# Optimization experiments

Measured on AMD Instinct MI355X. Metric: run time of the kernel, lower is better.

Reference implementation:

```python
import jax, jax.numpy as jnp
import numpy as np

N_NODES = 100000
IN_DIM = 128
HID_DIM = 128
N_EDGES = 1600000
BN_EPS = 1e-5


def setup_inputs() -> dict:
    key = jax.random.key(0)
    k1, k2, k3, k4 = jax.random.split(key, 4)
    x = jax.random.normal(k1, (N_NODES, IN_DIM), dtype=jnp.float32)
    edge_index = jax.random.randint(k2, (2, N_EDGES), 0, N_NODES, dtype=jnp.int64)
    # GCNConv linear weight (glorot) and bias
    W = jax.random.normal(k3, (HID_DIM, IN_DIM), dtype=jnp.float32) * (1.0 / np.sqrt(IN_DIM))
    b = jnp.zeros((HID_DIM,), dtype=jnp.float32)
    # BatchNorm affine params
    gamma = jnp.ones((HID_DIM,), dtype=jnp.float32)
    beta = jnp.zeros((HID_DIM,), dtype=jnp.float32)
    return {"x": x, "edge_index": edge_index, "W": W, "b": b, "gamma": gamma, "beta": beta}


def reference(x, edge_index, W, b, gamma, beta):
    n = x.shape[0]
    # --- GCNConv: add self loops, symmetric normalization ---
    loops = jnp.arange(n, dtype=edge_index.dtype)
    row = jnp.concatenate([edge_index[0], loops])  # source j
    col = jnp.concatenate([edge_index[1], loops])  # target i
    deg = jax.ops.segment_sum(jnp.ones_like(col, dtype=x.dtype), col, num_segments=n)
    deg_inv_sqrt = jnp.where(deg > 0, jax.lax.rsqrt(jnp.maximum(deg, 1e-12)), 0.0)
    norm = deg_inv_sqrt[row] * deg_inv_sqrt[col]  # [E+N]
    # linear transform then normalized gather-scatter aggregation
    h = x @ W.T  # [N, H]
    msgs = h[row] * norm[:, None]  # [E+N, H]
    out = jax.ops.segment_sum(msgs, col, num_segments=n) + b  # [N, H]
    # --- BatchNorm1d (training-mode batch stats, biased var) + ReLU ---
    mean = jnp.mean(out, axis=0)
    var = jnp.mean(jnp.square(out - mean), axis=0)
    out = (out - mean) * jax.lax.rsqrt(var + BN_EPS) * gamma + beta
    return jax.nn.relu(out)
```

## Files before the change

### kernel.cpp

```cpp
#include <hip/hip_runtime.h>

#define N_NODES 100000
#define N_EDGES 1600000
#define BN_EPS 1e-5f
#define SB 25
#define SCAP 69632
#define NBB 800
#define CAP 2688

typedef short short8 __attribute__((ext_vector_type(8)));
typedef float floatx4 __attribute__((ext_vector_type(4)));

__device__ __forceinline__ unsigned short f2bf(float f) {
    unsigned int u = __float_as_uint(f);
    unsigned int r = (u + 0x7fffu + ((u >> 16) & 1u)) >> 16;
    return (unsigned short)r;
}
__device__ __forceinline__ float bflo(unsigned int v) { return __uint_as_float(v << 16); }
__device__ __forceinline__ float bfhi(unsigned int v) { return __uint_as_float(v & 0xffff0000u); }

__global__ __launch_bounds__(512) void k_binA(const int* __restrict__ ei,
                                              int* __restrict__ scnt,
                                              unsigned int* __restrict__ b1, int E) {
    __shared__ int hist[32], base[32], gbase[32];
    __shared__ unsigned int stage[4096];
    __shared__ unsigned char stb[4096];
    int tid = threadIdx.x;
    int e0 = blockIdx.x * 4096;
    int cn = min(4096, E - e0);
    if (tid < 32) hist[tid] = 0;
    __syncthreads();

    unsigned int mycode[8];
    short myslot[8];
    signed char myb[8];
    #pragma unroll
    for (int j = 0; j < 8; j++) {
        int idx = j * 512 + tid;
        if (idx < cn) {
            int src = ei[e0 + idx];
            int dst = ei[E + e0 + idx];
            int s = dst >> 12;
            mycode[j] = (unsigned int)src | ((unsigned int)(dst & 4095) << 17);
            myb[j] = (signed char)s;
            myslot[j] = (short)atomicAdd(&hist[s], 1);
        } else myb[j] = -1;
    }
    __syncthreads();
    if (tid == 0) {
        int run = 0;
        for (int s = 0; s < SB; s++) { base[s] = run; run += hist[s]; }
    }
    __syncthreads();
    #pragma unroll
    for (int j = 0; j < 8; j++) {
        if (myb[j] >= 0) {
            int p = base[myb[j]] + myslot[j];
            stage[p] = mycode[j];
            stb[p] = (unsigned char)myb[j];
        }
    }
    if (tid < SB && hist[tid]) gbase[tid] = tid * SCAP + atomicAdd(&scnt[tid], hist[tid]);
    __syncthreads();
    for (int i = tid; i < cn; i += 512) {
        int s = stb[i];
        b1[gbase[s] + (i - base[s])] = stage[i];
    }
}

__global__ __launch_bounds__(512) void k_binB(const unsigned int* __restrict__ b1,
                                              const int* __restrict__ scnt,
                                              int* __restrict__ bcnt,
                                              unsigned int* __restrict__ b2) {
    __shared__ int hist[32], base[32], gbase[32];
    __shared__ unsigned int stage[4096];
    __shared__ unsigned char stb[4096];
    int tid = threadIdx.x;
    int s = blockIdx.x / 17;
    int c = blockIdx.x % 17;
    int cnt = scnt[s];
    int e0 = s * SCAP + c * 4096;
    int cn = min(4096, cnt - c * 4096);
    if (tid < 32) hist[tid] = 0;
    __syncthreads();

    unsigned int mycode[8];
    short myslot[8];
    signed char myb[8];
    #pragma unroll
    for (int j = 0; j < 8; j++) {
        int idx = j * 512 + tid;
        if (idx < cn) {
            unsigned int code = b1[e0 + idx];
            int sub = (code >> 24) & 31;
            mycode[j] = code & 0x00FFFFFFu;
            myb[j] = (signed char)sub;
            myslot[j] = (short)atomicAdd(&hist[sub], 1);
        } else myb[j] = -1;
    }
    __syncthreads();
    if (tid == 0) {
        int run = 0;
        for (int k = 0; k < 32; k++) { base[k] = run; run += hist[k]; }
    }
    __syncthreads();
    #pragma unroll
    for (int j = 0; j < 8; j++) {
        if (myb[j] >= 0) {
            int p = base[myb[j]] + myslot[j];
            stage[p] = mycode[j];
            stb[p] = (unsigned char)myb[j];
        }
    }
    if (tid < 32 && hist[tid]) {
        int gb = s * 32 + tid;
        gbase[tid] = gb * CAP + atomicAdd(&bcnt[gb], hist[tid]);
    }
    __syncthreads();
    for (int i = tid; i < cn; i += 512) {
        int sub = stb[i];
        b2[gbase[sub] + (i - base[sub])] = stage[i];
    }
}

__global__ __launch_bounds__(256) void k_dd(const unsigned int* __restrict__ binned,
                                            const int* __restrict__ bcnt,
                                            float* __restrict__ dinv, int n) {
    __shared__ int hist[128];
    int b = blockIdx.x, t = threadIdx.x;
    int nb0 = b * 128;
    int e0 = b * CAP;
    int cnt = bcnt[b];
    if (t < 128) hist[t] = 0;
    __syncthreads();
    for (int i = t; i < cnt; i += 256)
        atomicAdd(&hist[binned[e0 + i] >> 17], 1);
    __syncthreads();
    int nr = min(128, n - nb0);
    if (t < nr) dinv[nb0 + t] = rsqrtf((float)(hist[t] + 1));
}

__global__ void k_wcvt(const float* __restrict__ Wf, unsigned short* __restrict__ Wb) {
    int i = blockIdx.x * 256 + threadIdx.x;
    if (i < 128 * 128) Wb[i] = f2bf(Wf[i]);
}

__global__ __launch_bounds__(256) void k_gemm(const float* __restrict__ x,
                                              const unsigned short* __restrict__ Wb,
                                              const float* __restrict__ dinv,
                                              unsigned short* __restrict__ gb, int n) {
    int w = threadIdx.x >> 6;
    int l = threadIdx.x & 63;
    int rowbase = blockIdx.x * 128 + w * 32;
    int r16 = l & 15;
    int kg = l >> 4;

    short8 a[2][4];
    float dv[2][4];
    #pragma unroll
    for (int m = 0; m < 2; m++) {
        int row = rowbase + m * 16 + r16;
        int rca = min(row, n - 1);
        const float* base = x + rca * 128;
        #pragma unroll
        for (int q = 0; q < 4; q++) {
            const float4* xp = (const float4*)(base + q * 32 + kg * 8);
            float4 lo = xp[0], hi = xp[1];
            short8 af;
            af[0] = (short)f2bf(lo.x); af[1] = (short)f2bf(lo.y);
            af[2] = (short)f2bf(lo.z); af[3] = (short)f2bf(lo.w);
            af[4] = (short)f2bf(hi.x); af[5] = (short)f2bf(hi.y);
            af[6] = (short)f2bf(hi.z); af[7] = (short)f2bf(hi.w);
            a[m][q] = af;
        }
        #pragma unroll
        for (int r = 0; r < 4; r++)
            dv[m][r] = dinv[min(rowbase + m * 16 + kg * 4 + r, n - 1)];
    }
    for (int t = 0; t < 8; t++) {
        int col = t * 16 + r16;
        short8 b[4];
        #pragma unroll
        for (int q = 0; q < 4; q++)
            b[q] = *(const short8*)(Wb + col * 128 + q * 32 + kg * 8);

        floatx4 acc[2] = {};
        #pragma unroll
        for (int m = 0; m < 2; m++)
            #pragma unroll
            for (int q = 0; q < 4; q++)
                acc[m] = __builtin_amdgcn_mfma_f32_16x16x32_bf16(a[m][q], b[q], acc[m], 0, 0, 0);

        #pragma unroll
        for (int m = 0; m < 2; m++) {
            #pragma unroll
            for (int r = 0; r < 4; r++) {
                int row = rowbase + m * 16 + kg * 4 + r;
                if (row < n) gb[row * 128 + col] = f2bf(acc[m][r] * dv[m][r]);
            }
        }
    }
}

__global__ __launch_bounds__(512) void k_fused(const unsigned int* __restrict__ hp,
        const float* __restrict__ dinv, const int* __restrict__ bcnt,
        const unsigned int* __restrict__ binned, float* __restrict__ out,
        float* __restrict__ sums, float* __restrict__ sumsq, int n) {
    __shared__ int hist[128], hsc[128];
    __shared__ float dl[128];
    __shared__ unsigned int sh_src[CAP];
    __shared__ float ps[8][64], pq[8][64];
    int t = threadIdx.x;
    int w = t >> 6, l = t & 63;
    int bid = blockIdx.x;
    int b = bid >> 1;
    int ch = bid & 1;
    int half = l >> 5;
    int cu = ch * 32 + (l & 31);
    int nb0 = b * 128;
    int e0 = b * CAP;
    int cnt = bcnt[b];
    int nr = min(128, n - nb0);

    if (t < 128) {
        hist[t] = 0;
        if (t < nr) dl[t] = dinv[nb0 + t];
    }
    __syncthreads();

    unsigned int mycode[6];
    short myslot[6];
    #pragma unroll
    for (int j = 0; j < 6; j++) {
        int i = j * 512 + t;
        if (i < cnt) {
            unsigned int code = binned[e0 + i];
            mycode[j] = code;
            myslot[j] = (short)atomicAdd(&hist[code >> 17], 1);
        } else myslot[j] = -1;
    }
    __syncthreads();

    int v = (t < 128) ? hist[t] : 0;
    if (t < 128) hsc[t] = v;
    __syncthreads();
    for (int o = 1; o < 128; o <<= 1) {
        int x = (t < 128 && t >= o) ? hsc[t - o] : 0;
        __syncthreads();
        if (t < 128) hsc[t] += x;
        __syncthreads();
    }

    #pragma unroll
    for (int j = 0; j < 6; j++) {
        if (myslot[j] >= 0) {
            unsigned int code = mycode[j];
            int ld = code >> 17;
            int pos = hsc[ld] - hist[ld] + myslot[j];
            sh_src[pos] = code & 0x1FFFF;
        }
    }
    __syncthreads();

    float s0 = 0, s1 = 0, q0 = 0, q1 = 0;
    for (int r = w; r < nr; r += 8) {
        int i = nb0 + r;
        float di = dl[r];
        float ax = 0.f, ay = 0.f;
        int off = hsc[r] - hist[r];
        int dg = hist[r];
        int e = 0;
        for (; e + 15 < dg; e += 16) {
            unsigned int hv[8];
            #pragma unroll
            for (int j = 0; j < 8; j++)
                hv[j] = hp[sh_src[off + e + 2 * j + half] * 64 + cu];
            #pragma unroll
            for (int j = 0; j < 8; j++) {
                ax += bflo(hv[j]);
                ay += bfhi(hv[j]);
            }
        }
        for (; e + 3 < dg; e += 4) {
            unsigned int h0 = hp[sh_src[off + e + half] * 64 + cu];
            unsigned int h1 = hp[sh_src[off + e + 2 + half] * 64 + cu];
            ax += bflo(h0) + bflo(h1);
            ay += bfhi(h0) + bfhi(h1);
        }
        for (; e < dg; e += 2) {
            int idx = e + half;
            if (idx < dg) {
                unsigned int hv = hp[sh_src[off + idx] * 64 + cu];
                ax += bflo(hv);
                ay += bfhi(hv);
            }
        }
        ax += __shfl_xor(ax, 32);
        ay += __shfl_xor(ay, 32);
        if (half == 0) {
            unsigned int sv = hp[i * 64 + cu];
            float v0 = di * (ax + bflo(sv));
            float v1 = di * (ay + bfhi(sv));
            ((float2*)out)[i * 64 + cu] = make_float2(v0, v1);
            s0 += v0; q0 += v0 * v0;
            s1 += v1; q1 += v1 * v1;
        }
    }

    if (half == 0) {
        ps[w][2 * (l & 31)] = s0; ps[w][2 * (l & 31) + 1] = s1;
        pq[w][2 * (l & 31)] = q0; pq[w][2 * (l & 31) + 1] = q1;
    }
    __syncthreads();
    if (t < 64) {
        float s = 0, q = 0;
        #pragma unroll
        for (int j = 0; j < 8; j++) { s += ps[j][t]; q += pq[j][t]; }
        atomicAdd(&sums[ch * 64 + t], s);
        atomicAdd(&sumsq[ch * 64 + t], q);
    }
}

__global__ void k_bn(float* __restrict__ out, const float* __restrict__ sums,
                     const float* __restrict__ sumsq, const float* __restrict__ gamma,
                     const float* __restrict__ beta, int n) {
    int idx = blockIdx.x * 256 + threadIdx.x;
    int total = n * 32;
    if (idx >= total) return;
    int c0 = (idx & 31) * 4;
    float invN = 1.0f / (float)n;
    float4 v = ((const float4*)out)[idx];
    float r[4] = {v.x, v.y, v.z, v.w};
    #pragma unroll
    for (int j = 0; j < 4; j++) {
        int c = c0 + j;
        float mean = sums[c] * invN;
        float var = sumsq[c] * invN - mean * mean;
        float scale = rsqrtf(var + BN_EPS) * gamma[c];
        float o = (r[j] - mean) * scale + beta[c];
        r[j] = fmaxf(o, 0.0f);
    }
    ((float4*)out)[idx] = make_float4(r[0], r[1], r[2], r[3]);
}

extern "C" void kernel_launch(void* const* d_in, const int* in_sizes, int n_in,
                              void* d_out, int out_size, void* d_ws, size_t ws_size,
                              hipStream_t stream) {
    const float* x     = (const float*)d_in[0];
    const int*   ei    = (const int*)d_in[1];
    const float* W     = (const float*)d_in[2];
    const float* gamma = (const float*)d_in[4];
    const float* beta  = (const float*)d_in[5];
    float* out = (float*)d_out;

    const int n = N_NODES, E = N_EDGES;

    unsigned short* gbuf = (unsigned short*)d_ws;
    float* dinv   = (float*)(gbuf + 12800000);
    float* sums   = dinv + 100000;
    float* sumsq  = sums + 128;
    int*   bcnt   = (int*)(sumsq + 128);
    int*   scnt   = bcnt + NBB;
    unsigned short* Wb = (unsigned short*)(scnt + SB);
    unsigned int* b1 = (unsigned int*)(Wb + 16384);
    unsigned int* b2 = b1 + SB * SCAP;

    hipMemsetAsync(sums, 0, (256 + NBB + SB) * sizeof(int), stream);

    k_binA<<<(E + 4095) / 4096, 512, 0, stream>>>(ei, scnt, b1, E);
    k_binB<<<SB * 17, 512, 0, stream>>>(b1, scnt, bcnt, b2);
    k_dd<<<NBB, 256, 0, stream>>>(b2, bcnt, dinv, n);

    k_wcvt<<<64, 256, 0, stream>>>(W, Wb);
    k_gemm<<<(n + 127) / 128, 256, 0, stream>>>(x, Wb, dinv, gbuf, n);

    k_fused<<<NBB * 2, 512, 0, stream>>>((const unsigned int*)gbuf, dinv, bcnt, b2,
                                         out, sums, sumsq, n);

    k_bn<<<(n * 32 + 255) / 256, 256, 0, stream>>>(out, sums, sumsq, gamma, beta, n);
}
```

Baseline: 162.7 us.

## Build CSR in degree kernel and aggregate with small per-node blocks

The degree kernel now also performs the per-bucket counting sort in place and writes CSR offsets and degrees. The aggregation kernel drops its large shared-memory sort and runs one wavefront per node with 256-thread blocks, broadcasting source indices via shuffles. The aim is to raise occupancy and load balance in the gather. BatchNorm statistics move to a separate kernel, which costs an extra full read of the output.

```diff
diff --git a/kernel.cpp b/kernel.cpp
--- a/kernel.cpp
+++ b/kernel.cpp
@@ -123,21 +123,46 @@
     }
 }
 
-__global__ __launch_bounds__(256) void k_dd(const unsigned int* __restrict__ binned,
-                                            const int* __restrict__ bcnt,
-                                            float* __restrict__ dinv, int n) {
-    __shared__ int hist[128];
+__global__ __launch_bounds__(256) void k_sortd(unsigned int* __restrict__ b2,
+        const int* __restrict__ bcnt, int* __restrict__ offs, int* __restrict__ deg,
+        float* __restrict__ dinv, int n) {
+    __shared__ unsigned int stage[CAP];
+    __shared__ int hist[128], hsc[128];
     int b = blockIdx.x, t = threadIdx.x;
     int nb0 = b * 128;
     int e0 = b * CAP;
     int cnt = bcnt[b];
     if (t < 128) hist[t] = 0;
     __syncthreads();
-    for (int i = t; i < cnt; i += 256)
-        atomicAdd(&hist[binned[e0 + i] >> 17], 1);
-    __syncthreads();
+    for (int i = t; i < cnt; i += 256) {
+        unsigned int code = b2[e0 + i];
+        stage[i] = code;
+        atomicAdd(&hist[code >> 17], 1);
+    }
+    __syncthreads();
+    int v = (t < 128) ? hist[t] : 0;
+    if (t < 128) hsc[t] = v;
+    __syncthreads();
+    for (int o = 1; o < 128; o <<= 1) {
+        int x = (t < 128 && t >= o) ? hsc[t - o] : 0;
+        __syncthreads();
+        if (t < 128) hsc[t] += x;
+        __syncthreads();
+    }
     int nr = min(128, n - nb0);
-    if (t < nr) dinv[nb0 + t] = rsqrtf((float)(hist[t] + 1));
+    if (t < nr) {
+        int start = hsc[t] - v;
+        offs[nb0 + t] = e0 + start;
+        deg[nb0 + t] = v;
+        dinv[nb0 + t] = rsqrtf((float)(v + 1));
+        hist[t] = start;
+    }
+    __syncthreads();
+    for (int i = t; i < cnt; i += 256) {
+        unsigned int code = stage[i];
+        int pos = atomicAdd(&hist[code >> 17], 1);
+        b2[e0 + pos] = code & 0x1FFFF;
+    }
 }
 
 __global__ void k_wcvt(const float* __restrict__ Wf, unsigned short* __restrict__ Wb) {
@@ -202,122 +227,86 @@
     }
 }
 
-__global__ __launch_bounds__(512) void k_fused(const unsigned int* __restrict__ hp,
-        const float* __restrict__ dinv, const int* __restrict__ bcnt,
-        const unsigned int* __restrict__ binned, float* __restrict__ out,
-        float* __restrict__ sums, float* __restrict__ sumsq, int n) {
-    __shared__ int hist[128], hsc[128];
-    __shared__ float dl[128];
-    __shared__ unsigned int sh_src[CAP];
-    __shared__ float ps[8][64], pq[8][64];
+__global__ __launch_bounds__(256) void k_agg(const unsigned int* __restrict__ hp,
+        const float* __restrict__ dinv, const int* __restrict__ offs,
+        const int* __restrict__ deg, const unsigned int* __restrict__ csr,
+        float* __restrict__ out, int n) {
     int t = threadIdx.x;
     int w = t >> 6, l = t & 63;
     int bid = blockIdx.x;
-    int b = bid >> 1;
+    int nblk = bid >> 1;
     int ch = bid & 1;
     int half = l >> 5;
     int cu = ch * 32 + (l & 31);
-    int nb0 = b * 128;
-    int e0 = b * CAP;
-    int cnt = bcnt[b];
-    int nr = min(128, n - nb0);
-
-    if (t < 128) {
-        hist[t] = 0;
-        if (t < nr) dl[t] = dinv[nb0 + t];
-    }
-    __syncthreads();
-
-    unsigned int mycode[6];
-    short myslot[6];
-    #pragma unroll
-    for (int j = 0; j < 6; j++) {
-        int i = j * 512 + t;
-        if (i < cnt) {
-            unsigned int code = binned[e0 + i];
-            mycode[j] = code;
-            myslot[j] = (short)atomicAdd(&hist[code >> 17], 1);
-        } else myslot[j] = -1;
-    }
-    __syncthreads();
-
-    int v = (t < 128) ? hist[t] : 0;
-    if (t < 128) hsc[t] = v;
-    __syncthreads();
-    for (int o = 1; o < 128; o <<= 1) {
-        int x = (t < 128 && t >= o) ? hsc[t - o] : 0;
-        __syncthreads();
-        if (t < 128) hsc[t] += x;
-        __syncthreads();
-    }
-
-    #pragma unroll
-    for (int j = 0; j < 6; j++) {
-        if (myslot[j] >= 0) {
-            unsigned int code = mycode[j];
-            int ld = code >> 17;
-            int pos = hsc[ld] - hist[ld] + myslot[j];
-            sh_src[pos] = code & 0x1FFFF;
-        }
-    }
-    __syncthreads();
-
-    float s0 = 0, s1 = 0, q0 = 0, q1 = 0;
-    for (int r = w; r < nr; r += 8) {
-        int i = nb0 + r;
-        float di = dl[r];
-        float ax = 0.f, ay = 0.f;
-        int off = hsc[r] - hist[r];
-        int dg = hist[r];
+    int i = nblk * 4 + w;
+    if (i >= n) return;
+    float di = dinv[i];
+    int s0 = offs[i];
+    int dg = deg[i];
+    float ax = 0.f, ay = 0.f;
+    for (int base = 0; base < dg; base += 64) {
+        int rem = min(dg - base, 64);
+        unsigned int mysrc = (l < rem) ? csr[s0 + base + l] : 0;
         int e = 0;
-        for (; e + 15 < dg; e += 16) {
+        for (; e + 15 < rem; e += 16) {
             unsigned int hv[8];
             #pragma unroll
-            for (int j = 0; j < 8; j++)
-                hv[j] = hp[sh_src[off + e + 2 * j + half] * 64 + cu];
+            for (int j = 0; j < 8; j++) {
+                int s = __shfl(mysrc, e + 2 * j + half);
+                hv[j] = hp[s * 64 + cu];
+            }
             #pragma unroll
             for (int j = 0; j < 8; j++) {
                 ax += bflo(hv[j]);
                 ay += bfhi(hv[j]);
             }
         }
-        for (; e + 3 < dg; e += 4) {
-            unsigned int h0 = hp[sh_src[off + e + half] * 64 + cu];
-            unsigned int h1 = hp[sh_src[off + e + 2 + half] * 64 + cu];
-            ax += bflo(h0) + bflo(h1);
-            ay += bfhi(h0) + bfhi(h1);
-        }
-        for (; e < dg; e += 2) {
-            int idx = e + half;
-            if (idx < dg) {
-                unsigned int hv = hp[sh_src[off + idx] * 64 + cu];
+        for (; e + 1 < rem; e += 2) {
+            int s = __shfl(mysrc, e + half);
+            unsigned int hv = hp[s * 64 + cu];
+            ax += bflo(hv);
+            ay += bfhi(hv);
+        }
+        if (e < rem) {
+            int s = __shfl(mysrc, e);
+            if (half == 0) {
+                unsigned int hv = hp[s * 64 + cu];
                 ax += bflo(hv);
                 ay += bfhi(hv);
             }
         }
-        ax += __shfl_xor(ax, 32);
-        ay += __shfl_xor(ay, 32);
-        if (half == 0) {
-            unsigned int sv = hp[i * 64 + cu];
-            float v0 = di * (ax + bflo(sv));
-            float v1 = di * (ay + bfhi(sv));
-            ((float2*)out)[i * 64 + cu] = make_float2(v0, v1);
-            s0 += v0; q0 += v0 * v0;
-            s1 += v1; q1 += v1 * v1;
-        }
-    }
-
+    }
+    ax += __shfl_xor(ax, 32);
+    ay += __shfl_xor(ay, 32);
     if (half == 0) {
-        ps[w][2 * (l & 31)] = s0; ps[w][2 * (l & 31) + 1] = s1;
-        pq[w][2 * (l & 31)] = q0; pq[w][2 * (l & 31) + 1] = q1;
-    }
-    __syncthreads();
-    if (t < 64) {
+        unsigned int sv = hp[i * 64 + cu];
+        float v0 = di * (ax + bflo(sv));
+        float v1 = di * (ay + bfhi(sv));
+        ((float2*)out)[i * 64 + cu] = make_float2(v0, v1);
+    }
+}
+
+__global__ void k_stats(const float* __restrict__ out, float* __restrict__ sums,
+                        float* __restrict__ sumsq, int n) {
+    int tid = threadIdx.x;
+    int c2 = tid & 63;
+    int rh = tid >> 6;
+    float s0 = 0, s1 = 0, q0 = 0, q1 = 0;
+    for (int r = blockIdx.x * 4 + rh; r < n; r += gridDim.x * 4) {
+        float2 v = ((const float2*)out)[r * 64 + c2];
+        s0 += v.x; q0 += v.x * v.x;
+        s1 += v.y; q1 += v.y * v.y;
+    }
+    __shared__ float ls[4][128], lq[4][128];
+    ls[rh][2 * c2] = s0; ls[rh][2 * c2 + 1] = s1;
+    lq[rh][2 * c2] = q0; lq[rh][2 * c2 + 1] = q1;
+    __syncthreads();
+    if (tid < 128) {
         float s = 0, q = 0;
         #pragma unroll
-        for (int j = 0; j < 8; j++) { s += ps[j][t]; q += pq[j][t]; }
-        atomicAdd(&sums[ch * 64 + t], s);
-        atomicAdd(&sumsq[ch * 64 + t], q);
+        for (int j = 0; j < 4; j++) { s += ls[j][tid]; q += lq[j][tid]; }
+        atomicAdd(&sums[tid], s);
+        atomicAdd(&sumsq[tid], q);
     }
 }
 
@@ -357,7 +346,9 @@
 
     unsigned short* gbuf = (unsigned short*)d_ws;
     float* dinv   = (float*)(gbuf + 12800000);
-    float* sums   = dinv + 100000;
+    int*   offs   = (int*)(dinv + 100000);
+    int*   deg    = offs + 100000;
+    float* sums   = (float*)(deg + 100000);
     float* sumsq  = sums + 128;
     int*   bcnt   = (int*)(sumsq + 128);
     int*   scnt   = bcnt + NBB;
@@ -369,13 +360,14 @@
 
     k_binA<<<(E + 4095) / 4096, 512, 0, stream>>>(ei, scnt, b1, E);
     k_binB<<<SB * 17, 512, 0, stream>>>(b1, scnt, bcnt, b2);
-    k_dd<<<NBB, 256, 0, stream>>>(b2, bcnt, dinv, n);
+    k_sortd<<<NBB, 256, 0, stream>>>(b2, bcnt, offs, deg, dinv, n);
 
     k_wcvt<<<64, 256, 0, stream>>>(W, Wb);
     k_gemm<<<(n + 127) / 128, 256, 0, stream>>>(x, Wb, dinv, gbuf, n);
 
-    k_fused<<<NBB * 2, 512, 0, stream>>>((const unsigned int*)gbuf, dinv, bcnt, b2,
-                                         out, sums, sumsq, n);
-
+    k_agg<<<((n + 3) / 4) * 2, 256, 0, stream>>>((const unsigned int*)gbuf, dinv, offs, deg,
+                                                 (const unsigned int*)b2, out, n);
+
+    k_stats<<<512, 256, 0, stream>>>(out, sums, sumsq, n);
     k_bn<<<(n * 32 + 255) / 256, 256, 0, stream>>>(out, sums, sumsq, gamma, beta, n);
 }
```

After: 214.5 us. +31.8%, slower.
